# Kernel tuning notes

Measured on AMD Instinct MI355X. Metric: run time of the kernel, lower is better.

The kernel has to match this reference:

```python
import jax, jax.numpy as jnp
import numpy as np

N_NODES = 50000
N_EDGES = 800000
D = 128


def setup_inputs() -> dict:
    key = jax.random.key(0)
    k1, k2, k3, k4 = jax.random.split(key, 4)
    x = jax.random.normal(k1, (N_NODES, D), dtype=jnp.float32)
    src = jax.random.randint(k2, (N_EDGES,), 0, N_NODES, dtype=jnp.int64)
    dst = jax.random.randint(k3, (N_EDGES,), 0, N_NODES, dtype=jnp.int64)
    # nn.Linear(D, D, bias=False): weight shape [out, in]
    W = jax.random.normal(k4, (D, D), dtype=jnp.float32) * (1.0 / np.sqrt(D))
    return {"x": x, "src": src, "dst": dst, "W": W}


def reference(x, src, dst, W):
    h_in = x
    # update_all(copy_src, reduce_sum): gather src features, segment-sum over dst
    agg = jax.ops.segment_sum(x[src], dst, num_segments=N_NODES)  # [N, D]
    h = agg @ W.T                 # Linear(bias=False)
    h = jax.nn.relu(h)            # activation
    h = h + h_in                  # residual (is_normalize=False)
    return h
```

## Files before the change

kernel.cpp:

```cpp
#include <hip/hip_runtime.h>
#include <hip/hip_bf16.h>

#define N_NODES 50000
#define N_EDGES 800000
#define D 128

#define NBUCK 3125
#define BCAP  512

#define SCAT_BLOCKS ((N_EDGES / 4 + 1023) / 1024)

using bf16x8 = __attribute__((ext_vector_type(8))) short;
using u16x8  = __attribute__((ext_vector_type(8))) unsigned short;
using f32x4  = __attribute__((ext_vector_type(4))) float;

static __device__ __forceinline__ ushort f2bf(float f) {
    __hip_bfloat16 h = __float2bfloat16(f);
    return *reinterpret_cast<ushort*>(&h);
}
static __device__ __forceinline__ float bf2f(ushort u) {
    return __uint_as_float(((unsigned)u) << 16);
}


__global__ void __launch_bounds__(1024)
convert_scatter(const float4* __restrict__ x4, ushort* __restrict__ xb,
                const float* __restrict__ W, ushort* __restrict__ wb,
                const int* __restrict__ src, const int* __restrict__ dst,
                int* __restrict__ bcnt, int* __restrict__ pairs) {
    __shared__ int lcnt[NBUCK], lbase[NBUCK];
    const int tid = threadIdx.x;
    for (int t0 = tid; t0 < NBUCK; t0 += 1024) lcnt[t0] = 0;

    const int i = blockIdx.x * 1024 + tid;
    const bool valid = i < N_EDGES / 4;
    int4 s, d;
    if (valid) {
        s = ((const int4*)src)[i];
        d = ((const int4*)dst)[i];
    }

    const int g = blockIdx.x * 1024 + tid;
    if (g < 2048) {
        int o  = g & 127;
        int kc = g >> 7;
        const float4* wp = (const float4*)(W + (size_t)o * D + kc * 8);
        float4 w0 = wp[0], w1 = wp[1];
        bf16x8 hv;
        hv[0] = (short)f2bf(w0.x); hv[1] = (short)f2bf(w0.y);
        hv[2] = (short)f2bf(w0.z); hv[3] = (short)f2bf(w0.w);
        hv[4] = (short)f2bf(w1.x); hv[5] = (short)f2bf(w1.y);
        hv[6] = (short)f2bf(w1.z); hv[7] = (short)f2bf(w1.w);
        *(bf16x8*)&wb[g * 8] = hv;
    }

    const int total4 = N_NODES * D / 4;
    const int stride = gridDim.x * 1024;
    for (int j = blockIdx.x * 1024 + tid; j < total4; j += stride) {
        float4 v = x4[j];
        ushort4 u = make_ushort4(f2bf(v.x), f2bf(v.y), f2bf(v.z), f2bf(v.w));
        *(ushort4*)(xb + (size_t)j * 4) = u;
    }
    __syncthreads();

    int bkt[4], slot[4];
    if (valid) {
        bkt[0] = d.x >> 4; slot[0] = atomicAdd(&lcnt[bkt[0]], 1);
        bkt[1] = d.y >> 4; slot[1] = atomicAdd(&lcnt[bkt[1]], 1);
        bkt[2] = d.z >> 4; slot[2] = atomicAdd(&lcnt[bkt[2]], 1);
        bkt[3] = d.w >> 4; slot[3] = atomicAdd(&lcnt[bkt[3]], 1);
    }
    __syncthreads();
    for (int t0 = tid; t0 < NBUCK; t0 += 1024) {
        int c = lcnt[t0];
        lbase[t0] = c ? atomicAdd(&bcnt[t0], c) : 0;
    }
    __syncthreads();
    if (valid) {
#pragma unroll
        for (int e = 0; e < 4; ++e) {
            int sv = (e == 0) ? s.x : (e == 1) ? s.y : (e == 2) ? s.z : s.w;
            int dv = (e == 0) ? d.x : (e == 1) ? d.y : (e == 2) ? d.z : d.w;
            int pos = lbase[bkt[e]] + slot[e];
            if (pos < BCAP)
                pairs[bkt[e] * BCAP + pos] = sv | ((dv & 15) << 16);
        }
    }
}

__global__ void __launch_bounds__(256)
csr_gather_gemm(const int* __restrict__ pairs, const int* __restrict__ bcnt,
                const ushort* __restrict__ xb, const ushort* __restrict__ wb,
                float* __restrict__ out) {
    __shared__ __align__(16) char lds[14016];
    ushort* lsrc  = (ushort*)lds;
    ushort* aggL  = (ushort*)(lds + 1024);
    float*  Ew    = (float*)(lds + 5376);
    int*    lcnt2 = (int*)(lds + 13824);
    int*    lcur  = (int*)(lds + 13888);
    int*    lbeg  = (int*)(lds + 13952);

    const int b    = blockIdx.x;
    const int tid  = threadIdx.x;
    const int lane = tid & 63;
    const int wv   = tid >> 6;
    const int m16  = lane & 15;
    const int q    = lane >> 4;

    const int base = b * BCAP;
    int n = bcnt[b];
    if (n > BCAP) n = BCAP;
    if (tid < 16) lcnt2[tid] = 0;
    __syncthreads();
    for (int i = tid; i < n; i += 256)
        atomicAdd(&lcnt2[pairs[base + i] >> 16], 1);
    __syncthreads();
    if (tid < 16) {
        int v = lcnt2[tid];
        int incl = v;
#pragma unroll
        for (int o = 1; o < 16; o <<= 1) {
            int t = __shfl_up(incl, o, 64);
            if (tid >= o) incl += t;
        }
        lbeg[tid] = incl - v;
        lcur[tid] = incl - v;
    }
    __syncthreads();
    for (int i = tid; i < n; i += 256) {
        int p = pairs[base + i];
        int pos = atomicAdd(&lcur[p >> 16], 1);
        lsrc[pos] = (ushort)(p & 0xFFFF);
    }
    __syncthreads();

    const int c8 = m16 << 3;
    const ushort* xbb = xb + c8;
#pragma unroll 1
    for (int m = 0; m < 4; ++m) {
        const int nloc = wv * 4 + m;
        const int beg = lbeg[nloc], end = lcur[nloc];
        float acc[8];
#pragma unroll
        for (int j = 0; j < 8; ++j) acc[j] = 0.f;

        int t = beg;
        for (; t + 16 <= end; t += 16) {
            int s0 = lsrc[t + q];
            int s1 = lsrc[t + 4 + q];
            int s2 = lsrc[t + 8 + q];
            int s3 = lsrc[t + 12 + q];
            u16x8 u0 = *(const u16x8*)(xbb + (size_t)s0 * D);
            u16x8 u1 = *(const u16x8*)(xbb + (size_t)s1 * D);
            u16x8 u2 = *(const u16x8*)(xbb + (size_t)s2 * D);
            u16x8 u3 = *(const u16x8*)(xbb + (size_t)s3 * D);
#pragma unroll
            for (int j = 0; j < 8; ++j)
                acc[j] += (bf2f(u0[j]) + bf2f(u1[j])) + (bf2f(u2[j]) + bf2f(u3[j]));
        }
        for (; t + 4 <= end; t += 4) {
            int s = lsrc[t + q];
            u16x8 u = *(const u16x8*)(xbb + (size_t)s * D);
#pragma unroll
            for (int j = 0; j < 8; ++j) acc[j] += bf2f(u[j]);
        }
        const int rem = end - t;
        if (rem && q < rem) {
            int s = lsrc[t + q];
            u16x8 u = *(const u16x8*)(xbb + (size_t)s * D);
#pragma unroll
            for (int j = 0; j < 8; ++j) acc[j] += bf2f(u[j]);
        }
#pragma unroll
        for (int j = 0; j < 8; ++j) {
            acc[j] += __shfl_xor(acc[j], 16, 64);
            acc[j] += __shfl_xor(acc[j], 32, 64);
        }
        if (q == 0) {
            u16x8 u;
#pragma unroll
            for (int j = 0; j < 8; ++j) u[j] = f2bf(acc[j]);
            *(u16x8*)&aggL[(size_t)nloc * 136 + c8] = u;
        }
    }
    __syncthreads();

    bf16x8 a[4];
#pragma unroll
    for (int kb = 0; kb < 4; ++kb)
        a[kb] = *(const bf16x8*)&aggL[(size_t)m16 * 136 + kb * 32 + q * 8];

    f32x4 acc[2];
#pragma unroll
    for (int tt = 0; tt < 2; ++tt) {
        const int t = wv * 2 + tt;
        acc[tt] = (f32x4){0.f, 0.f, 0.f, 0.f};
#pragma unroll
        for (int kb = 0; kb < 4; ++kb) {
            bf16x8 bfr = *(const bf16x8*)&wb[(((kb * 4 + q) * 128) + t * 16 + m16) * 8];
            acc[tt] = __builtin_amdgcn_mfma_f32_16x16x32_bf16(a[kb], bfr, acc[tt], 0, 0, 0);
        }
    }

#pragma unroll
    for (int tt = 0; tt < 2; ++tt) {
        const int t = wv * 2 + tt;
#pragma unroll
        for (int r = 0; r < 4; ++r)
            Ew[(q * 4 + r) * 132 + t * 16 + m16] = acc[tt][r];
    }
    __syncthreads();

#pragma unroll
    for (int k = 0; k < 2; ++k) {
        int idx = tid + k * 256;
        int row = idx >> 5;
        int c4  = (idx & 31) << 2;
        int node = b * 16 + row;
        float4 v  = *(const float4*)&Ew[row * 132 + c4];
        ushort4 xu = *(const ushort4*)(xb + (size_t)node * D + c4);
        float4 o;
        o.x = fmaxf(v.x, 0.f) + bf2f(xu.x);
        o.y = fmaxf(v.y, 0.f) + bf2f(xu.y);
        o.z = fmaxf(v.z, 0.f) + bf2f(xu.z);
        o.w = fmaxf(v.w, 0.f) + bf2f(xu.w);
        *(float4*)(out + (size_t)node * D + c4) = o;
    }
}

__global__ void zero_out(float4* __restrict__ p, int n4) {
    int i = blockIdx.x * 256 + threadIdx.x;
    if (i < n4) p[i] = make_float4(0.f, 0.f, 0.f, 0.f);
}
__global__ void scatter_edges(const float* __restrict__ x,
                              const int* __restrict__ src,
                              const int* __restrict__ dst,
                              float* __restrict__ agg) {
    long long tid = (long long)blockIdx.x * 256 + threadIdx.x;
    if (tid >= (long long)N_EDGES * 32) return;
    int edge = (int)(tid >> 5);
    int c    = ((int)tid & 31) << 2;
    const float4 v = *(const float4*)(x + (size_t)src[edge] * D + c);
    float* p = agg + (size_t)dst[edge] * D + c;
    unsafeAtomicAdd(p + 0, v.x);
    unsafeAtomicAdd(p + 1, v.y);
    unsafeAtomicAdd(p + 2, v.z);
    unsafeAtomicAdd(p + 3, v.w);
}
__global__ void __launch_bounds__(256)
gemm_relu_res_f32(float* data, const float* __restrict__ W,
                  const float* __restrict__ x) {
    __shared__ __align__(16) char lds[50176];
    ushort* Wl = (ushort*)lds;
    ushort* Al = (ushort*)(lds + 32768);
    const int tid  = threadIdx.x;
    const int lane = tid & 63;
    const int wv   = tid >> 6;
    const int m16  = lane & 15;
    const int q    = lane >> 4;
#pragma unroll
    for (int i = 0; i < 8; ++i) {
        int g  = tid + i * 256;
        int o  = g & 127;
        int kc = g >> 7;
        const float4* wp = (const float4*)(W + (size_t)o * D + kc * 8);
        float4 w0 = wp[0], w1 = wp[1];
        bf16x8 hv;
        hv[0] = (short)f2bf(w0.x); hv[1] = (short)f2bf(w0.y);
        hv[2] = (short)f2bf(w0.z); hv[3] = (short)f2bf(w0.w);
        hv[4] = (short)f2bf(w1.x); hv[5] = (short)f2bf(w1.y);
        hv[6] = (short)f2bf(w1.z); hv[7] = (short)f2bf(w1.w);
        *(bf16x8*)&Wl[g * 8] = hv;
    }
    __syncthreads();
    const int nb = blockIdx.x * 64 + wv * 16;
    ushort* Aw = &Al[wv * (16 * 136)];
#pragma unroll
    for (int m = 0; m < 16; ++m) {
        int node = nb + m;
        float2 v = make_float2(0.f, 0.f);
        if (node < N_NODES)
            v = *(const float2*)(data + (size_t)node * D + lane * 2);
        *(ushort2*)&Aw[m * 136 + lane * 2] = make_ushort2(f2bf(v.x), f2bf(v.y));
    }
    bf16x8 a[4];
#pragma unroll
    for (int kb = 0; kb < 4; ++kb)
        a[kb] = *(const bf16x8*)&Aw[m16 * 136 + kb * 32 + q * 8];
    f32x4 acc[8];
#pragma unroll
    for (int t = 0; t < 8; ++t) {
        acc[t] = (f32x4){0.f, 0.f, 0.f, 0.f};
#pragma unroll
        for (int kb = 0; kb < 4; ++kb) {
            bf16x8 bfr = *(const bf16x8*)&Wl[(((kb * 4 + q) * 128) + t * 16 + m16) * 8];
            acc[t] = __builtin_amdgcn_mfma_f32_16x16x32_bf16(a[kb], bfr, acc[t], 0, 0, 0);
        }
    }
    __syncthreads();
    float* Ew = (float*)(lds + wv * 8448);
#pragma unroll
    for (int t = 0; t < 8; ++t)
#pragma unroll
        for (int r = 0; r < 4; ++r)
            Ew[(q * 4 + r) * 132 + t * 16 + m16] = acc[t][r];
    const int h  = lane >> 5;
    const int c4 = (lane & 31) << 2;
#pragma unroll
    for (int j = 0; j < 8; ++j) {
        int r = j * 2 + h;
        int node = nb + r;
        if (node < N_NODES) {
            float4 v  = *(const float4*)&Ew[r * 132 + c4];
            float4 xi = *(const float4*)(x + (size_t)node * D + c4);
            float4 o;
            o.x = fmaxf(v.x, 0.f) + xi.x;
            o.y = fmaxf(v.y, 0.f) + xi.y;
            o.z = fmaxf(v.z, 0.f) + xi.z;
            o.w = fmaxf(v.w, 0.f) + xi.w;
            *(float4*)(data + (size_t)node * D + c4) = o;
        }
    }
}

extern "C" void kernel_launch(void* const* d_in, const int* in_sizes, int n_in,
                              void* d_out, int out_size, void* d_ws, size_t ws_size,
                              hipStream_t stream) {
    const float* x   = (const float*)d_in[0];
    const int*   src = (const int*)d_in[1];
    const int*   dst = (const int*)d_in[2];
    const float* W   = (const float*)d_in[3];
    float* out = (float*)d_out;

    char* ws = (char*)d_ws;
    int*    bcnt  = (int*)ws;        ws += (size_t)NBUCK * 4;
    ws = (char*)(((uintptr_t)ws + 15) & ~(uintptr_t)15);
    int*    pairs = (int*)ws;        ws += (size_t)NBUCK * BCAP * 4;
    ushort* xb    = (ushort*)ws;     ws += (size_t)N_NODES * D * 2;
    ushort* wb    = (ushort*)ws;     ws += (size_t)D * D * 2;
    const bool big_ws = (ws_size >= (size_t)(ws - (char*)d_ws));

    if (big_ws) {
        hipMemsetAsync(bcnt, 0, (size_t)NBUCK * 4, stream);
        convert_scatter<<<SCAT_BLOCKS, 1024, 0, stream>>>(
            (const float4*)x, xb, W, wb, src, dst, bcnt, pairs);
        csr_gather_gemm<<<NBUCK, 256, 0, stream>>>(pairs, bcnt, xb, wb, out);
    } else {
        int n4 = N_NODES * D / 4;
        zero_out<<<(n4 + 255) / 256, 256, 0, stream>>>((float4*)out, n4);
        long long n_scatter = (long long)N_EDGES * 32;
        scatter_edges<<<(int)((n_scatter + 255) / 256), 256, 0, stream>>>(
            x, src, dst, out);
        gemm_relu_res_f32<<<(N_NODES + 63) / 64, 256, 0, stream>>>(out, W, x);
    }
}
```

Before: 137.3 us.

## Replace block-local LDS bucket histogram with direct global atomics in scatter

The scatter kernel drops its per-block LDS histogram, the three block barriers and the per-bucket global reservation, and instead does one global atomicAdd per edge into the bucket counters. It now launches 3200 blocks of 256 threads, with x conversion in a grid-stride loop. The aim is to avoid a large LDS footprint and barrier stalls and to let the conversion overlap with the scatter. In exchange it issues four times more global atomics, spread over 3125 counters, and bucket slot order becomes nondeterministic. The gather kernel also loads each thread's two pairs into registers once and reuses them for the count and placement passes instead of reading them twice.

After: 195.2 us. +42.1%, slower.

```diff
diff --git a/kernel.cpp b/kernel.cpp
--- a/kernel.cpp
+++ b/kernel.cpp
@@ -8,7 +8,7 @@
 #define NBUCK 3125
 #define BCAP  512
 
-#define SCAT_BLOCKS ((N_EDGES / 4 + 1023) / 1024)
+#define CONV_BLOCKS 3200
 
 using bf16x8 = __attribute__((ext_vector_type(8))) short;
 using u16x8  = __attribute__((ext_vector_type(8))) unsigned short;
@@ -23,27 +23,16 @@
 }
 
 
-__global__ void __launch_bounds__(1024)
+__global__ void __launch_bounds__(256)
 convert_scatter(const float4* __restrict__ x4, ushort* __restrict__ xb,
                 const float* __restrict__ W, ushort* __restrict__ wb,
                 const int* __restrict__ src, const int* __restrict__ dst,
                 int* __restrict__ bcnt, int* __restrict__ pairs) {
-    __shared__ int lcnt[NBUCK], lbase[NBUCK];
-    const int tid = threadIdx.x;
-    for (int t0 = tid; t0 < NBUCK; t0 += 1024) lcnt[t0] = 0;
-
-    const int i = blockIdx.x * 1024 + tid;
-    const bool valid = i < N_EDGES / 4;
-    int4 s, d;
-    if (valid) {
-        s = ((const int4*)src)[i];
-        d = ((const int4*)dst)[i];
-    }
-
-    const int g = blockIdx.x * 1024 + tid;
-    if (g < 2048) {
-        int o  = g & 127;
-        int kc = g >> 7;
+    const int gt = blockIdx.x * 256 + threadIdx.x;
+
+    if (gt < 2048) {
+        int o  = gt & 127;
+        int kc = gt >> 7;
         const float4* wp = (const float4*)(W + (size_t)o * D + kc * 8);
         float4 w0 = wp[0], w1 = wp[1];
         bf16x8 hv;
@@ -51,40 +40,29 @@
         hv[2] = (short)f2bf(w0.z); hv[3] = (short)f2bf(w0.w);
         hv[4] = (short)f2bf(w1.x); hv[5] = (short)f2bf(w1.y);
         hv[6] = (short)f2bf(w1.z); hv[7] = (short)f2bf(w1.w);
-        *(bf16x8*)&wb[g * 8] = hv;
+        *(bf16x8*)&wb[gt * 8] = hv;
+    }
+
+    if (gt < N_EDGES / 4) {
+        int4 s = ((const int4*)src)[gt];
+        int4 d = ((const int4*)dst)[gt];
+#pragma unroll
+        for (int e = 0; e < 4; ++e) {
+            int sv = (e == 0) ? s.x : (e == 1) ? s.y : (e == 2) ? s.z : s.w;
+            int dv = (e == 0) ? d.x : (e == 1) ? d.y : (e == 2) ? d.z : d.w;
+            int bkt = dv >> 4;
+            int pos = atomicAdd(&bcnt[bkt], 1);
+            if (pos < BCAP)
+                pairs[bkt * BCAP + pos] = sv | ((dv & 15) << 16);
+        }
     }
 
     const int total4 = N_NODES * D / 4;
-    const int stride = gridDim.x * 1024;
-    for (int j = blockIdx.x * 1024 + tid; j < total4; j += stride) {
+    const int stride = CONV_BLOCKS * 256;
+    for (int j = gt; j < total4; j += stride) {
         float4 v = x4[j];
         ushort4 u = make_ushort4(f2bf(v.x), f2bf(v.y), f2bf(v.z), f2bf(v.w));
         *(ushort4*)(xb + (size_t)j * 4) = u;
-    }
-    __syncthreads();
-
-    int bkt[4], slot[4];
-    if (valid) {
-        bkt[0] = d.x >> 4; slot[0] = atomicAdd(&lcnt[bkt[0]], 1);
-        bkt[1] = d.y >> 4; slot[1] = atomicAdd(&lcnt[bkt[1]], 1);
-        bkt[2] = d.z >> 4; slot[2] = atomicAdd(&lcnt[bkt[2]], 1);
-        bkt[3] = d.w >> 4; slot[3] = atomicAdd(&lcnt[bkt[3]], 1);
-    }
-    __syncthreads();
-    for (int t0 = tid; t0 < NBUCK; t0 += 1024) {
-        int c = lcnt[t0];
-        lbase[t0] = c ? atomicAdd(&bcnt[t0], c) : 0;
-    }
-    __syncthreads();
-    if (valid) {
-#pragma unroll
-        for (int e = 0; e < 4; ++e) {
-            int sv = (e == 0) ? s.x : (e == 1) ? s.y : (e == 2) ? s.z : s.w;
-            int dv = (e == 0) ? d.x : (e == 1) ? d.y : (e == 2) ? d.z : d.w;
-            int pos = lbase[bkt[e]] + slot[e];
-            if (pos < BCAP)
-                pairs[bkt[e] * BCAP + pos] = sv | ((dv & 15) << 16);
-        }
     }
 }
 
@@ -110,10 +88,13 @@
     const int base = b * BCAP;
     int n = bcnt[b];
     if (n > BCAP) n = BCAP;
+    int p0 = -1, p1 = -1;
+    if (tid < n)       p0 = pairs[base + tid];
+    if (tid + 256 < n) p1 = pairs[base + 256 + tid];
     if (tid < 16) lcnt2[tid] = 0;
     __syncthreads();
-    for (int i = tid; i < n; i += 256)
-        atomicAdd(&lcnt2[pairs[base + i] >> 16], 1);
+    if (p0 >= 0) atomicAdd(&lcnt2[p0 >> 16], 1);
+    if (p1 >= 0) atomicAdd(&lcnt2[p1 >> 16], 1);
     __syncthreads();
     if (tid < 16) {
         int v = lcnt2[tid];
@@ -127,10 +108,13 @@
         lcur[tid] = incl - v;
     }
     __syncthreads();
-    for (int i = tid; i < n; i += 256) {
-        int p = pairs[base + i];
-        int pos = atomicAdd(&lcur[p >> 16], 1);
-        lsrc[pos] = (ushort)(p & 0xFFFF);
+    if (p0 >= 0) {
+        int pos = atomicAdd(&lcur[p0 >> 16], 1);
+        lsrc[pos] = (ushort)(p0 & 0xFFFF);
+    }
+    if (p1 >= 0) {
+        int pos = atomicAdd(&lcur[p1 >> 16], 1);
+        lsrc[pos] = (ushort)(p1 & 0xFFFF);
     }
     __syncthreads();
 
@@ -342,7 +326,7 @@
 
     if (big_ws) {
         hipMemsetAsync(bcnt, 0, (size_t)NBUCK * 4, stream);
-        convert_scatter<<<SCAT_BLOCKS, 1024, 0, stream>>>(
+        convert_scatter<<<CONV_BLOCKS, 256, 0, stream>>>(
             (const float4*)x, xb, W, wb, src, dst, bcnt, pairs);
         csr_gather_gemm<<<NBUCK, 256, 0, stream>>>(pairs, bcnt, xb, wb, out);
     } else {
```
